# Kernel tuning notes

Hardware: AMD Instinct MI355X
Metric: run time of the kernel (lower is better)

Reference implementation:

```python
import jax, jax.numpy as jnp
import numpy as np

D_MODEL = 256
NHEAD = 8
NLAYERS = 4
B, L, K = 8, 4096, 10
EPS_ATT = 1e-6
EPS_LN = 1e-5
EPS_COS = 1e-8


def setup_inputs() -> dict:
    key = jax.random.key(0)
    ks = jax.random.split(key, 12)
    s = 1.0 / np.sqrt(D_MODEL)
    s2 = 1.0 / np.sqrt(2 * D_MODEL)
    return {
        "ClassNum": K,
        "feat": jax.random.normal(ks[0], (B, L, D_MODEL), jnp.float32),
        "feat_class": jax.random.normal(ks[1], (B, K, D_MODEL), jnp.float32),
        "Wq": jax.random.normal(ks[2], (NLAYERS, D_MODEL, D_MODEL), jnp.float32) * s,
        "Wk": jax.random.normal(ks[3], (NLAYERS, D_MODEL, D_MODEL), jnp.float32) * s,
        "Wv": jax.random.normal(ks[4], (NLAYERS, D_MODEL, D_MODEL), jnp.float32) * s,
        "Wm": jax.random.normal(ks[5], (NLAYERS, D_MODEL, D_MODEL), jnp.float32) * s,
        "W1": jax.random.normal(ks[6], (NLAYERS, 2 * D_MODEL, 2 * D_MODEL), jnp.float32) * s2,
        "W2": jax.random.normal(ks[7], (NLAYERS, 2 * D_MODEL, D_MODEL), jnp.float32) * s2,
        "g1": jnp.ones((NLAYERS, D_MODEL), jnp.float32),
        "b1": jnp.zeros((NLAYERS, D_MODEL), jnp.float32),
        "g2": jnp.ones((NLAYERS, D_MODEL), jnp.float32),
        "b2": jnp.zeros((NLAYERS, D_MODEL), jnp.float32),
    }


def _layernorm(x, g, b):
    mu = jnp.mean(x, axis=-1, keepdims=True)
    xc = x - mu
    var = jnp.mean(xc * xc, axis=-1, keepdims=True)
    return g * xc * jax.lax.rsqrt(var + EPS_LN) + b


def _encoder_layer(x, oh, Wq, Wk, Wv, Wm, W1, W2, g1, b1, g2, b2):
    # x: [B,L,C], oh: [B,L,K] one-hot cluster assignment.
    # Per-cluster LoFTR linear self-attention via segment sums (exact: the
    # per-cluster v_length scaling in LinearAttention cancels algebraically).
    bsz, seq, cdim = x.shape
    hd = cdim // NHEAD
    q = (x @ Wq).reshape(bsz, seq, NHEAD, hd)
    k = (x @ Wk).reshape(bsz, seq, NHEAD, hd)
    v = (x @ Wv).reshape(bsz, seq, NHEAD, hd)
    Q = jax.nn.elu(q) + 1.0
    Kf = jax.nn.elu(k) + 1.0
    # per-(batch,cluster) sums: KV [B,K,H,D,D], Ksum [B,K,H,D]
    KV = jnp.einsum('blc,blhd,blhe->bchde', oh, Kf, v)
    Ksum = jnp.einsum('blc,blhd->bchd', oh, Kf)
    Kt = jnp.einsum('blc,bchd->blhd', oh, Ksum)  # cluster ΣK gathered per token
    Z = 1.0 / (jnp.einsum('blhd,blhd->blh', Q, Kt) + EPS_ATT)
    msg = jnp.zeros((bsz, seq, NHEAD, hd), x.dtype)
    for c in range(oh.shape[-1]):  # small fixed ClassNum loop
        msg = msg + oh[:, :, c][:, :, None, None] * jnp.einsum(
            'blhd,bhde->blhe', Q, KV[:, c])
    msg = msg * Z[..., None]
    m = msg.reshape(bsz, seq, cdim) @ Wm
    m = _layernorm(m, g1, b1)
    h = jnp.concatenate([x, m], axis=-1) @ W1
    h = jax.nn.relu(h) @ W2
    m = _layernorm(h, g2, b2)
    return x + m


def reference(ClassNum, feat, feat_class, Wq, Wk, Wv, Wm, W1, W2, g1, b1, g2, b2):
    x = jax.lax.stop_gradient(feat)          # feat.clone().detach()
    fc = jax.lax.stop_gradient(feat_class)   # feat_class.clone().detach()
    # cosine-similarity top-1 cluster routing (torch.F.cosine_similarity, eps=1e-8)
    na = jnp.linalg.norm(fc, axis=-1)  # [B,K]
    nb = jnp.linalg.norm(x, axis=-1)   # [B,L]
    dot = jnp.einsum('bkc,blc->bkl', fc, x)
    sim = dot / jnp.maximum(na[:, :, None] * nb[:, None, :], EPS_COS)
    seg = jnp.argmax(sim, axis=1)  # [B,L] cluster id per token
    oh = jax.nn.one_hot(seg, ClassNum, dtype=x.dtype)
    for li in range(Wq.shape[0]):
        x = _encoder_layer(x, oh, Wq[li], Wk[li], Wv[li], Wm[li],
                           W1[li], W2[li], g1[li], b1[li], g2[li], b2[li])
    return x
```

## Files before the change

kernel.cpp:

```cpp
#include <hip/hip_runtime.h>
#include <hip/hip_bf16.h>
#include <math.h>

#define DM 256
#define NHEAD 8
#define HD 32
#define NL 4
#define BATCH 8
#define SEQ 4096
#define KCLS 10
#define M_TOK (BATCH*SEQ)

#define BKG 64

#define PADPOS 5120
#define NWIN (PADPOS/64)
#define KVWIN 20
#define NGRP (KVWIN*4)

using bf16x8 = __attribute__((ext_vector_type(8))) short;
using f32x4  = __attribute__((ext_vector_type(4))) float;

__device__ __forceinline__ unsigned short f2bf(float f) {
    __hip_bfloat16 b = __float2bfloat16(f);
    return __builtin_bit_cast(unsigned short, b);
}
__device__ __forceinline__ float bf2f(unsigned short u) {
    unsigned v = (unsigned)u << 16;
    return __builtin_bit_cast(float, v);
}

__device__ __forceinline__ float wave_reduce_sum(float v) {
    #pragma unroll
    for (int off = 32; off > 0; off >>= 1) v += __shfl_xor(v, off, 64);
    return v;
}

__global__ __launch_bounds__(64) void fcn_kernel(const float* __restrict__ fc,
                                                 float* __restrict__ fcn) {
    int bk = blockIdx.x;
    int lane = threadIdx.x;
    float4 fv = *(const float4*)(fc + (size_t)bk * DM + lane * 4);
    float n = fv.x*fv.x + fv.y*fv.y + fv.z*fv.z + fv.w*fv.w;
    n = wave_reduce_sum(n);
    if (lane == 0) fcn[bk] = sqrtf(n);
}

__global__ void route_kernel(const float* __restrict__ feat, const float* __restrict__ fc,
                             const float* __restrict__ fcn,
                             float* __restrict__ x, unsigned short* __restrict__ xm,
                             int* __restrict__ seg) {
    int wid = (int)((blockIdx.x * (size_t)blockDim.x + threadIdx.x) >> 6);
    int lane = threadIdx.x & 63;
    if (wid >= M_TOK) return;
    int b = wid / SEQ;
    float4 xv = *(const float4*)(feat + (size_t)wid * DM + lane * 4);
    *(float4*)(x + (size_t)wid * DM + lane * 4) = xv;
    ushort4 u; u.x = f2bf(xv.x); u.y = f2bf(xv.y); u.z = f2bf(xv.z); u.w = f2bf(xv.w);
    *(ushort4*)(xm + (size_t)wid * 512 + lane * 4) = u;
    float nb2 = xv.x*xv.x + xv.y*xv.y + xv.z*xv.z + xv.w*xv.w;
    nb2 = wave_reduce_sum(nb2);
    float nb = sqrtf(nb2);
    float best = -1e30f; int bestk = 0;
    for (int k = 0; k < KCLS; ++k) {
        float4 fv = *(const float4*)(fc + ((size_t)(b * KCLS + k)) * DM + lane * 4);
        float d = fv.x*xv.x + fv.y*xv.y + fv.z*xv.z + fv.w*xv.w;
        d = wave_reduce_sum(d);
        float sim = d / fmaxf(fcn[b * KCLS + k] * nb, 1e-8f);
        if (sim > best) { best = sim; bestk = k; }
    }
    if (lane == 0) seg[wid] = bestk;
}

__global__ __launch_bounds__(256) void seg_count(const int* __restrict__ seg,
                                                 int* __restrict__ cnt) {
    __shared__ int wc[4][KCLS];
    int b = blockIdx.x >> 4, chunk = blockIdx.x & 15;
    int t = threadIdx.x, w = t >> 6, lane = t & 63;
    int c = seg[b * SEQ + chunk * 256 + t];
    #pragma unroll
    for (int cc = 0; cc < KCLS; ++cc) {
        unsigned long long m = __ballot(c == cc);
        if (lane == 0) wc[w][cc] = __popcll(m);
    }
    __syncthreads();
    if (t < KCLS)
        cnt[(b * 16 + chunk) * KCLS + t] = wc[0][t] + wc[1][t] + wc[2][t] + wc[3][t];
}

__global__ __launch_bounds__(256) void seg_scan(const int* __restrict__ cnt,
                                                int* __restrict__ chunkbase,
                                                int* __restrict__ wseg,
                                                int* __restrict__ psegp,
                                                int* __restrict__ grange,
                                                int* __restrict__ prange,
                                                int* __restrict__ pidxp) {
    __shared__ int sTot[BATCH][KCLS];
    __shared__ int sBase[BATCH][KCLS];
    int tid = threadIdx.x;
    if (tid < BATCH * KCLS) {
        int b = tid / KCLS, c = tid % KCLS;
        int run = 0;
        #pragma unroll
        for (int j = 0; j < 16; ++j) run += cnt[(b * 16 + j) * KCLS + c];
        sTot[b][c] = run;
    }
    __syncthreads();
    if (tid < BATCH) {
        int b = tid, pb = 0;
        for (int c = 0; c < KCLS; ++c) {
            sBase[b][c] = pb;
            int psz = (sTot[b][c] + 63) & ~63;
            grange[(b * KCLS + c) * 2]     = pb >> 6;
            grange[(b * KCLS + c) * 2 + 1] = (pb + psz) >> 6;
            prange[(b * KCLS + c) * 2]     = pb + sTot[b][c];
            prange[(b * KCLS + c) * 2 + 1] = pb + psz;
            int w0 = pb >> 6, w1 = (pb + psz) >> 6;
            for (int w = w0; w < w1; ++w) wseg[b * NWIN + w] = c;
            pb += psz;
        }
        for (int w = pb >> 6; w < NWIN; ++w) wseg[b * NWIN + w] = -1;
    }
    __syncthreads();
    for (int i = tid; i < BATCH * PADPOS; i += 256) {
        int b = i / PADPOS, pos = i % PADPOS;
        int c = KCLS - 1;
        #pragma unroll
        for (int cc = KCLS - 1; cc >= 1; --cc)
            if (pos < sBase[b][cc]) c = cc - 1;
        psegp[i] = c;
        pidxp[i] = -1;
    }
    if (tid < BATCH * KCLS) {
        int b = tid / KCLS, c = tid % KCLS;
        int pre = 0;
        #pragma unroll
        for (int j = 0; j < 16; ++j) {
            chunkbase[(b * 16 + j) * KCLS + c] = sBase[b][c] + pre;
            pre += cnt[(b * 16 + j) * KCLS + c];
        }
    }
}

__global__ __launch_bounds__(256) void seg_scatter(const int* __restrict__ seg,
                                                   const int* __restrict__ chunkbase,
                                                   int* __restrict__ pidxp,
                                                   int* __restrict__ sortposG) {
    __shared__ int wc[4][KCLS];
    int b = blockIdx.x >> 4, chunk = blockIdx.x & 15;
    int t = threadIdx.x, w = t >> 6, lane = t & 63;
    int l = chunk * 256 + t;
    int c = seg[b * SEQ + l];
    int rank_w = 0;
    #pragma unroll
    for (int cc = 0; cc < KCLS; ++cc) {
        unsigned long long m = __ballot(c == cc);
        if (lane == 0) wc[w][cc] = __popcll(m);
        if (cc == c) rank_w = __popcll(m & ((1ULL << lane) - 1ULL));
    }
    __syncthreads();
    int rank = rank_w;
    for (int wp = 0; wp < 4; ++wp)
        if (wp < w) rank += wc[wp][c];
    int pos = chunkbase[(b * 16 + chunk) * KCLS + c] + rank;
    pidxp[b * PADPOS + pos] = l;
    sortposG[b * SEQ + l] = b * PADPOS + pos;
}

__global__ __launch_bounds__(256) void zero_pads(const int* __restrict__ prange,
                                                 unsigned short* __restrict__ Kb,
                                                 unsigned short* __restrict__ Vb) {
    int bc = blockIdx.x;
    int b = bc / KCLS;
    int ps = prange[bc * 2], pe = prange[bc * 2 + 1];
    int nrows = pe - ps;
    int t = threadIdx.x;
    bf16x8 z = (bf16x8){0,0,0,0,0,0,0,0};
    for (int idx = t; idx < nrows * 32; idx += 256) {
        int r = idx >> 5, c8 = (idx & 31) * 8;
        size_t row = (size_t)b * PADPOS + ps + r;
        *(bf16x8*)(Kb + row * DM + c8) = z;
        *(bf16x8*)(Vb + row * DM + c8) = z;
    }
}

__global__ __launch_bounds__(256) void transpose_all(
    const float* __restrict__ Wq, const float* __restrict__ Wk,
    const float* __restrict__ Wv, const float* __restrict__ Wm,
    const float* __restrict__ W1, const float* __restrict__ W2,
    unsigned short* __restrict__ WqkvT, unsigned short* __restrict__ WmT,
    unsigned short* __restrict__ W1T, unsigned short* __restrict__ W2T)
{
    __shared__ float s[64][65];
    int bid = blockIdx.x;
    int li = bid / 160, r = bid % 160;
    const float* src; unsigned short* dst; int K, N, kx, ny;
    if (r < 64) {
        int which = r >> 4, idx = r & 15;
        K = 256; N = 256; kx = idx & 3; ny = idx >> 2;
        if (which == 0)      { src = Wq + (size_t)li*65536; dst = WqkvT + (size_t)li*768*256; }
        else if (which == 1) { src = Wk + (size_t)li*65536; dst = WqkvT + (size_t)li*768*256 + 65536; }
        else if (which == 2) { src = Wv + (size_t)li*65536; dst = WqkvT + (size_t)li*768*256 + 131072; }
        else                 { src = Wm + (size_t)li*65536; dst = WmT + (size_t)li*65536; }
    } else if (r < 128) {
        int idx = r - 64;
        K = 512; N = 512; kx = idx & 7; ny = idx >> 3;
        src = W1 + (size_t)li*262144; dst = W1T + (size_t)li*262144;
    } else {
        int idx = r - 128;
        K = 512; N = 256; kx = idx & 7; ny = idx >> 3;
        src = W2 + (size_t)li*131072; dst = W2T + (size_t)li*131072;
    }
    int k0 = kx * 64, n0 = ny * 64;
    int t = threadIdx.x;
    int rr = t >> 4, c4 = (t & 15) * 4;
    #pragma unroll
    for (int i = 0; i < 4; ++i) {
        float4 v = *(const float4*)(src + (size_t)(k0 + rr + i*16) * N + n0 + c4);
        s[c4+0][rr+i*16] = v.x; s[c4+1][rr+i*16] = v.y;
        s[c4+2][rr+i*16] = v.z; s[c4+3][rr+i*16] = v.w;
    }
    __syncthreads();
    #pragma unroll
    for (int i = 0; i < 4; ++i) {
        int nr = rr + i*16;
        ushort4 u;
        u.x = f2bf(s[nr][c4+0]); u.y = f2bf(s[nr][c4+1]);
        u.z = f2bf(s[nr][c4+2]); u.w = f2bf(s[nr][c4+3]);
        *(ushort4*)(dst + (size_t)(n0 + nr) * K + k0 + c4) = u;
    }
}

template<int KD, int AS, int MODE>
__global__ __launch_bounds__(512, 4) void mfma_gemm(
    const unsigned short* __restrict__ A, const unsigned short* __restrict__ Bt,
    const int* __restrict__ sortpos,
    unsigned short* __restrict__ Ob0, unsigned short* __restrict__ Ob1,
    unsigned short* __restrict__ Ob2)
{
    __shared__ unsigned short As[128 * BKG];
    __shared__ unsigned short Bs[256 * BKG];
    __shared__ int sPos[128];
    int t = threadIdx.x;
    int lane = t & 63;
    int w = t >> 6;
    int wm = w & 1, wn = w >> 1;
    int li = lane & 15, lg = lane >> 4;
    int bm = blockIdx.x * 128;
    int bn = blockIdx.y * 256;

    if (MODE == 1 && t < 128) sPos[t] = sortpos[bm + t];

    f32x4 acc[4][4];
    #pragma unroll
    for (int m = 0; m < 4; ++m)
        #pragma unroll
        for (int n = 0; n < 4; ++n)
            acc[m][n] = (f32x4){0.f, 0.f, 0.f, 0.f};

    for (int k0 = 0; k0 < KD; k0 += BKG) {
        #pragma unroll
        for (int i = 0; i < 2; ++i) {
            int chunk = i * 512 + t;
            int row = chunk >> 3, cc = chunk & 7;
            int scc = cc ^ (row & 7);
            __builtin_amdgcn_global_load_lds(
                (const __attribute__((address_space(1))) void*)(A + (size_t)(bm + row) * AS + k0 + scc * 8),
                (__attribute__((address_space(3))) void*)((char*)As + chunk * 16), 16, 0, 0);
        }
        #pragma unroll
        for (int i = 0; i < 4; ++i) {
            int chunk = i * 512 + t;
            int row = chunk >> 3, cc = chunk & 7;
            int scc = cc ^ (row & 7);
            __builtin_amdgcn_global_load_lds(
                (const __attribute__((address_space(1))) void*)(Bt + (size_t)(bn + row) * KD + k0 + scc * 8),
                (__attribute__((address_space(3))) void*)((char*)Bs + chunk * 16), 16, 0, 0);
        }
        asm volatile("s_waitcnt vmcnt(0)");
        __syncthreads();
        #pragma unroll
        for (int kk = 0; kk < 2; ++kk) {
            int jc = kk * 4 + lg;
            bf16x8 af[4], bfr[4];
            #pragma unroll
            for (int m = 0; m < 4; ++m) {
                int R = wm*64 + m*16 + li;
                af[m] = *(const bf16x8*)((const char*)As + R * 128 + ((jc ^ (R & 7)) << 4));
            }
            #pragma unroll
            for (int n = 0; n < 4; ++n) {
                int R = wn*64 + n*16 + li;
                bfr[n] = *(const bf16x8*)((const char*)Bs + R * 128 + ((jc ^ (R & 7)) << 4));
            }
            #pragma unroll
            for (int m = 0; m < 4; ++m)
                #pragma unroll
                for (int n = 0; n < 4; ++n)
                    acc[m][n] = __builtin_amdgcn_mfma_f32_16x16x32_bf16(af[m], bfr[n], acc[m][n], 0, 0, 0);
        }
        __syncthreads();
    }

    int lrow0 = wm * 64 + (lane >> 4) * 4;
    int lcol = wn * 64 + (lane & 15);
    if (MODE == 1) {
        unsigned short* Obuf = (bn < 256) ? Ob0 : (bn < 512) ? Ob1 : Ob2;
        const bool act = (bn < 512);
        #pragma unroll
        for (int m = 0; m < 4; ++m)
            #pragma unroll
            for (int n = 0; n < 4; ++n)
                #pragma unroll
                for (int j = 0; j < 4; ++j) {
                    float v = acc[m][n][j];
                    if (act) v = (v > 0.f) ? v + 1.f : expf(v);
                    int drow = sPos[lrow0 + m*16 + j];
                    Obuf[(size_t)drow * 256 + lcol + n*16] = f2bf(v);
                }
    } else {
        #pragma unroll
        for (int m = 0; m < 4; ++m)
            #pragma unroll
            for (int n = 0; n < 4; ++n)
                #pragma unroll
                for (int j = 0; j < 4; ++j)
                    Ob0[(size_t)(bm + lrow0 + m*16 + j) * 512 + bn + lcol + n*16] =
                        f2bf(fmaxf(acc[m][n][j], 0.f));
    }
}

template<int KD, int LNMODE>
__global__ __launch_bounds__(256) void gemm_ln(
    const unsigned short* __restrict__ A, const unsigned short* __restrict__ Bt,
    const float* __restrict__ g, const float* __restrict__ bb,
    float* __restrict__ x, unsigned short* __restrict__ xm)
{
    __shared__ unsigned short As[64 * BKG];
    __shared__ unsigned short Bs[256 * BKG];
    __shared__ float redS[4][64];
    __shared__ float redQ[4][64];
    int t = threadIdx.x;
    int lane = t & 63;
    int w = t >> 6;
    int li = lane & 15, lg = lane >> 4;
    int bm = blockIdx.x * 64;

    f32x4 acc[4][4];
    #pragma unroll
    for (int m = 0; m < 4; ++m)
        #pragma unroll
        for (int n = 0; n < 4; ++n)
            acc[m][n] = (f32x4){0.f, 0.f, 0.f, 0.f};

    for (int k0 = 0; k0 < KD; k0 += BKG) {
        #pragma unroll
        for (int i = 0; i < 2; ++i) {
            int chunk = i * 256 + t;
            int row = chunk >> 3, cc = chunk & 7;
            int scc = cc ^ (row & 7);
            __builtin_amdgcn_global_load_lds(
                (const __attribute__((address_space(1))) void*)(A + (size_t)(bm + row) * KD + k0 + scc * 8),
                (__attribute__((address_space(3))) void*)((char*)As + chunk * 16), 16, 0, 0);
        }
        #pragma unroll
        for (int i = 0; i < 8; ++i) {
            int chunk = i * 256 + t;
            int row = chunk >> 3, cc = chunk & 7;
            int scc = cc ^ (row & 7);
            __builtin_amdgcn_global_load_lds(
                (const __attribute__((address_space(1))) void*)(Bt + (size_t)row * KD + k0 + scc * 8),
                (__attribute__((address_space(3))) void*)((char*)Bs + chunk * 16), 16, 0, 0);
        }
        asm volatile("s_waitcnt vmcnt(0)");
        __syncthreads();
        #pragma unroll
        for (int kk = 0; kk < 2; ++kk) {
            int jc = kk * 4 + lg;
            bf16x8 af[4], bfr[4];
            #pragma unroll
            for (int m = 0; m < 4; ++m) {
                int R = m*16 + li;
                af[m] = *(const bf16x8*)((const char*)As + R * 128 + ((jc ^ (R & 7)) << 4));
            }
            #pragma unroll
            for (int n = 0; n < 4; ++n) {
                int R = w*64 + n*16 + li;
                bfr[n] = *(const bf16x8*)((const char*)Bs + R * 128 + ((jc ^ (R & 7)) << 4));
            }
            #pragma unroll
            for (int m = 0; m < 4; ++m)
                #pragma unroll
                for (int n = 0; n < 4; ++n)
                    acc[m][n] = __builtin_amdgcn_mfma_f32_16x16x32_bf16(af[m], bfr[n], acc[m][n], 0, 0, 0);
        }
        __syncthreads();
    }

    float vs[4][4], vq[4][4];
    #pragma unroll
    for (int m = 0; m < 4; ++m)
        #pragma unroll
        for (int j = 0; j < 4; ++j) {
            float s = 0.f, q = 0.f;
            #pragma unroll
            for (int n = 0; n < 4; ++n) {
                float v = acc[m][n][j];
                s += v; q += v * v;
            }
            #pragma unroll
            for (int msk = 1; msk < 16; msk <<= 1) {
                s += __shfl_xor(s, msk, 64);
                q += __shfl_xor(q, msk, 64);
            }
            vs[m][j] = s; vq[m][j] = q;
        }
    if (li == 0) {
        #pragma unroll
        for (int m = 0; m < 4; ++m)
            #pragma unroll
            for (int j = 0; j < 4; ++j) {
                redS[w][m*16 + lg*4 + j] = vs[m][j];
                redQ[w][m*16 + lg*4 + j] = vq[m][j];
            }
    }
    __syncthreads();

    float gv[4], bv[4];
    #pragma unroll
    for (int n = 0; n < 4; ++n) {
        int col = w*64 + n*16 + li;
        gv[n] = g[col]; bv[n] = bb[col];
    }
    #pragma unroll
    for (int m = 0; m < 4; ++m)
        #pragma unroll
        for (int j = 0; j < 4; ++j) {
            int r = m*16 + lg*4 + j;
            float S = redS[0][r] + redS[1][r] + redS[2][r] + redS[3][r];
            float Q = redQ[0][r] + redQ[1][r] + redQ[2][r] + redQ[3][r];
            float mu = S * (1.f / 256.f);
            float var = Q * (1.f / 256.f) - mu * mu;
            float rs = rsqrtf(var + 1e-5f);
            #pragma unroll
            for (int n = 0; n < 4; ++n) {
                int col = w*64 + n*16 + li;
                float o = gv[n] * (acc[m][n][j] - mu) * rs + bv[n];
                if (LNMODE == 1) {
                    xm[(size_t)(bm + r) * 512 + 256 + col] = f2bf(o);
                } else {
                    size_t idx = (size_t)(bm + r) * 256 + col;
                    float xv = x[idx] + o;
                    x[idx] = xv;
                    xm[(size_t)(bm + r) * 512 + col] = f2bf(xv);
                }
            }
        }
}

__global__ __launch_bounds__(256) void kv_kernel(
    const unsigned short* __restrict__ Ksrt, const unsigned short* __restrict__ Vsrt,
    float* __restrict__ part)
{
    __shared__ float sK[64 * 33];
    __shared__ float sV[64 * 33];
    int blk = blockIdx.x;
    int s = blk % KVWIN;
    int bh = blk / KVWIN;
    int b = bh >> 3, h = bh & 7;
    int t = threadIdx.x;
    int d = t >> 3, e0 = (t & 7) * 4;
    int srow = t >> 2, soff = (t & 3) * 8;
    const size_t rowbase = (size_t)(b * PADPOS + s * 256);
    float* pball = part + ((size_t)bh * NGRP + s * 4) * 1056;

    for (int g = 0; g < 4; ++g) {
        size_t gsrc = (rowbase + g * 64 + srow) * DM + h * HD + soff;
        bf16x8 k8 = *(const bf16x8*)(Ksrt + gsrc);
        bf16x8 v8 = *(const bf16x8*)(Vsrt + gsrc);
        float4 ka, kb, va, vb;
        ka.x = bf2f((unsigned short)k8[0]); ka.y = bf2f((unsigned short)k8[1]);
        ka.z = bf2f((unsigned short)k8[2]); ka.w = bf2f((unsigned short)k8[3]);
        kb.x = bf2f((unsigned short)k8[4]); kb.y = bf2f((unsigned short)k8[5]);
        kb.z = bf2f((unsigned short)k8[6]); kb.w = bf2f((unsigned short)k8[7]);
        va.x = bf2f((unsigned short)v8[0]); va.y = bf2f((unsigned short)v8[1]);
        va.z = bf2f((unsigned short)v8[2]); va.w = bf2f((unsigned short)v8[3]);
        vb.x = bf2f((unsigned short)v8[4]); vb.y = bf2f((unsigned short)v8[5]);
        vb.z = bf2f((unsigned short)v8[6]); vb.w = bf2f((unsigned short)v8[7]);
        *(float4*)(sK + srow * 33 + soff)     = ka;
        *(float4*)(sK + srow * 33 + soff + 4) = kb;
        *(float4*)(sV + srow * 33 + soff)     = va;
        *(float4*)(sV + srow * 33 + soff + 4) = vb;
        __syncthreads();

        float4 a = {0.f, 0.f, 0.f, 0.f};
        float ks = 0.f;
        #pragma unroll 8
        for (int l = 0; l < 64; ++l) {
            float kd = sK[l * 33 + d];
            float4 v4 = *(const float4*)(sV + l * 33 + e0);
            a.x = fmaf(kd, v4.x, a.x);
            a.y = fmaf(kd, v4.y, a.y);
            a.z = fmaf(kd, v4.z, a.z);
            a.w = fmaf(kd, v4.w, a.w);
            ks += kd;
        }
        float* pb = pball + g * 1056;
        *(float4*)(pb + d * 32 + e0) = a;
        if ((t & 7) == 0) pb[1024 + d] = ks;
        __syncthreads();
    }
}

__global__ __launch_bounds__(256) void kv_reduce(
    const float* __restrict__ part, const int* __restrict__ grange,
    float* __restrict__ KV, float* __restrict__ Ks)
{
    int blk = blockIdx.x;
    int c = blk % KCLS;
    int bh = blk / KCLS;
    int b = bh >> 3, h = bh & 7;
    int t = threadIdx.x;
    const float* pb = part + (size_t)bh * NGRP * 1056;
    int g0 = grange[(b * KCLS + c) * 2];
    int g1 = grange[(b * KCLS + c) * 2 + 1];
    float4 acc = {0, 0, 0, 0};
    float ka = 0.f;
    for (int gg = g0; gg < g1; ++gg) {
        float4 v = *(const float4*)(pb + (size_t)gg * 1056 + t * 4);
        acc.x += v.x; acc.y += v.y; acc.z += v.z; acc.w += v.w;
        if (t < 32) ka += pb[(size_t)gg * 1056 + 1024 + t];
    }
    *(float4*)(KV + ((size_t)(b * KCLS + c) * NHEAD + h) * HD * HD + t * 4) = acc;
    if (t < 32) Ks[((size_t)(b * KCLS + c) * NHEAD + h) * HD + t] = ka;
}

__global__ __launch_bounds__(256) void msg_kernel(
    const unsigned short* __restrict__ Qs, const float* __restrict__ KV,
    const float* __restrict__ Ks, const int* __restrict__ pidxp,
    const int* __restrict__ wseg, unsigned short* __restrict__ msgb)
{
    int b = blockIdx.x / NWIN, w = blockIdx.x % NWIN;
    int c = wseg[b * NWIN + w];
    if (c < 0) return;
    __shared__ unsigned short sQ[64 * DM];
    __shared__ unsigned short kvT[NHEAD * HD * HD];
    __shared__ float sKs[NHEAD * HD];
    __shared__ float zl[64 * NHEAD];
    __shared__ int sTok[64];
    int t = threadIdx.x;
    int wv = t >> 6, lane = t & 63;

    if (t < 64) sTok[t] = pidxp[b * PADPOS + w * 64 + t];
    { int h = t >> 5, d = t & 31;
      sKs[h * HD + d] = Ks[((size_t)(b * KCLS + c) * NHEAD + h) * HD + d]; }
    const float* kvsrc = KV + (size_t)(b * KCLS + c) * NHEAD * HD * HD;
    #pragma unroll
    for (int i = 0; i < 8; ++i) {
        int q = i * 256 + t;
        float4 v = ((const float4*)kvsrc)[q];
        int g = q * 4;
        int h = g >> 10, rem = g & 1023;
        int d = rem >> 5, e = rem & 31;
        kvT[h * 1024 + (e + 0) * 32 + d] = f2bf(v.x);
        kvT[h * 1024 + (e + 1) * 32 + d] = f2bf(v.y);
        kvT[h * 1024 + (e + 2) * 32 + d] = f2bf(v.z);
        kvT[h * 1024 + (e + 3) * 32 + d] = f2bf(v.w);
    }
    const unsigned short* qsrc = Qs + (size_t)(b * PADPOS + w * 64) * DM;
    #pragma unroll
    for (int i = 0; i < 8; ++i) {
        int q = i * 256 + t;
        *(bf16x8*)(sQ + q * 8) = *(const bf16x8*)(qsrc + q * 8);
    }
    __syncthreads();

    #pragma unroll
    for (int i = 0; i < 2; ++i) {
        int idx = i * 256 + t;
        int r = idx >> 3, h = idx & 7;
        float z = 0.f;
        #pragma unroll
        for (int d8 = 0; d8 < 4; ++d8) {
            bf16x8 qv = *(const bf16x8*)(sQ + r * DM + h * 32 + d8 * 8);
            #pragma unroll
            for (int j = 0; j < 8; ++j)
                z = fmaf(bf2f((unsigned short)qv[j]), sKs[h * HD + d8 * 8 + j], z);
        }
        zl[r * NHEAD + h] = z;
    }
    __syncthreads();

    int li = lane & 15, lg = lane >> 4;
    #pragma unroll
    for (int hh = 0; hh < 2; ++hh) {
        int h = wv * 2 + hh;
        f32x4 acc[4][2];
        #pragma unroll
        for (int m = 0; m < 4; ++m)
            #pragma unroll
            for (int n = 0; n < 2; ++n)
                acc[m][n] = (f32x4){0.f, 0.f, 0.f, 0.f};
        bf16x8 bfr[2];
        #pragma unroll
        for (int n = 0; n < 2; ++n)
            bfr[n] = *(const bf16x8*)(kvT + h * 1024 + (n * 16 + li) * 32 + lg * 8);
        #pragma unroll
        for (int m = 0; m < 4; ++m) {
            bf16x8 af = *(const bf16x8*)(sQ + (m * 16 + li) * DM + h * 32 + lg * 8);
            #pragma unroll
            for (int n = 0; n < 2; ++n)
                acc[m][n] = __builtin_amdgcn_mfma_f32_16x16x32_bf16(af, bfr[n], acc[m][n], 0, 0, 0);
        }
        #pragma unroll
        for (int m = 0; m < 4; ++m)
            #pragma unroll
            for (int n = 0; n < 2; ++n)
                #pragma unroll
                for (int j = 0; j < 4; ++j) {
                    int r = m * 16 + lg * 4 + j;
                    int tok = sTok[r];
                    if (tok >= 0) {
                        float o = acc[m][n][j] / (zl[r * NHEAD + h] + 1e-6f);
                        msgb[(size_t)(b * SEQ + tok) * DM + h * 32 + n * 16 + li] = f2bf(o);
                    }
                }
    }
}

extern "C" void kernel_launch(void* const* d_in, const int* in_sizes, int n_in,
                              void* d_out, int out_size, void* d_ws, size_t ws_size,
                              hipStream_t stream)
{
    const float* feat = (const float*)d_in[1];
    const float* fc   = (const float*)d_in[2];
    const float* Wq   = (const float*)d_in[3];
    const float* Wk   = (const float*)d_in[4];
    const float* Wv   = (const float*)d_in[5];
    const float* Wm   = (const float*)d_in[6];
    const float* W1   = (const float*)d_in[7];
    const float* W2   = (const float*)d_in[8];
    const float* g1   = (const float*)d_in[9];
    const float* b1   = (const float*)d_in[10];
    const float* g2   = (const float*)d_in[11];
    const float* b2   = (const float*)d_in[12];
    float* x = (float*)d_out;

    char* ws = (char*)d_ws;
    auto alloc = [&](size_t bytes) { char* p = ws; ws += (bytes + 255) & ~(size_t)255; return p; };
    int*   seg    = (int*)  alloc((size_t)M_TOK * 4);
    int*   cnt    = (int*)  alloc((size_t)BATCH * 16 * KCLS * 4);
    int*   cbase  = (int*)  alloc((size_t)BATCH * 16 * KCLS * 4);
    int*   pidxp  = (int*)  alloc((size_t)BATCH * PADPOS * 4);
    int*   psegp  = (int*)  alloc((size_t)BATCH * PADPOS * 4);
    int*   sortposG = (int*)alloc((size_t)M_TOK * 4);
    int*   wseg   = (int*)  alloc((size_t)BATCH * NWIN * 4);
    int*   grange = (int*)  alloc((size_t)BATCH * KCLS * 2 * 4);
    int*   prange = (int*)  alloc((size_t)BATCH * KCLS * 2 * 4);
    float* fcn    = (float*)alloc((size_t)BATCH * KCLS * 4);
    float* KV     = (float*)alloc((size_t)BATCH * KCLS * NHEAD * HD * HD * 4);
    float* Ks     = (float*)alloc((size_t)BATCH * KCLS * NHEAD * HD * 4);
    unsigned short* xm = (unsigned short*)alloc((size_t)M_TOK * 512 * 2);
    char* bufA = alloc((size_t)M_TOK * 512 * 2);
    unsigned short* Qs   = (unsigned short*)alloc((size_t)BATCH * PADPOS * DM * 2);
    unsigned short* Ksrt = (unsigned short*)alloc((size_t)BATCH * PADPOS * DM * 2);
    unsigned short* Vsrt = (unsigned short*)alloc((size_t)BATCH * PADPOS * DM * 2);
    unsigned short* WqkvT = (unsigned short*)alloc((size_t)NL * 768 * 256 * 2);
    unsigned short* WmT   = (unsigned short*)alloc((size_t)NL * 256 * 256 * 2);
    unsigned short* W1T   = (unsigned short*)alloc((size_t)NL * 512 * 512 * 2);
    unsigned short* W2T   = (unsigned short*)alloc((size_t)NL * 256 * 512 * 2);

    unsigned short* hb   = (unsigned short*)bufA;
    unsigned short* msgb = (unsigned short*)bufA;
    float*          part = (float*)bufA;

    transpose_all<<<NL * 160, 256, 0, stream>>>(Wq, Wk, Wv, Wm, W1, W2,
                                                WqkvT, WmT, W1T, W2T);

    fcn_kernel<<<BATCH * KCLS, 64, 0, stream>>>(fc, fcn);
    route_kernel<<<8192, 256, 0, stream>>>(feat, fc, fcn, x, xm, seg);

    seg_count<<<BATCH * 16, 256, 0, stream>>>(seg, cnt);
    seg_scan<<<1, 256, 0, stream>>>(cnt, cbase, wseg, psegp, grange, prange, pidxp);
    seg_scatter<<<BATCH * 16, 256, 0, stream>>>(seg, cbase, pidxp, sortposG);
    zero_pads<<<BATCH * KCLS, 256, 0, stream>>>(prange, Ksrt, Vsrt);

    for (int li = 0; li < NL; ++li) {
        const unsigned short* wqkv = WqkvT + (size_t)li * 768 * 256;
        const unsigned short* wm   = WmT + (size_t)li * 65536;
        const unsigned short* w1   = W1T + (size_t)li * 262144;
        const unsigned short* w2   = W2T + (size_t)li * 131072;

        mfma_gemm<256, 512, 1><<<dim3(256, 3), 512, 0, stream>>>(xm, wqkv, sortposG, Qs, Ksrt, Vsrt);

        kv_kernel<<<BATCH * NHEAD * KVWIN, 256, 0, stream>>>(Ksrt, Vsrt, part);
        kv_reduce<<<BATCH * NHEAD * KCLS, 256, 0, stream>>>(part, grange, KV, Ks);

        msg_kernel<<<BATCH * NWIN, 256, 0, stream>>>(Qs, KV, Ks, pidxp, wseg, msgb);

        gemm_ln<256, 1><<<512, 256, 0, stream>>>(msgb, wm, g1 + li * DM, b1 + li * DM, nullptr, xm);

        mfma_gemm<512, 512, 2><<<dim3(256, 2), 512, 0, stream>>>(xm, w1, nullptr, hb, nullptr, nullptr);

        gemm_ln<512, 2><<<512, 256, 0, stream>>>(hb, w2, g2 + li * DM, b2 + li * DM, x, xm);
    }
}
```

Measured before the change: 646.9 us.

## Double-buffer LDS tiles in MFMA GEMM to overlap global loads with compute

Turns the GEMM's single shared-memory A/B tiles into two ping-pong buffers. The next K-slice is loaded straight into LDS while MFMAs run on the current slice, with one barrier per step instead of two. This is meant to hide global-load latency behind compute. It doubles LDS use per block (about 96KB+), which may cut the number of resident blocks below the launch-bounds target of 4.

```diff
diff --git a/kernel.cpp b/kernel.cpp
--- a/kernel.cpp
+++ b/kernel.cpp
@@ -238,8 +238,8 @@
     unsigned short* __restrict__ Ob0, unsigned short* __restrict__ Ob1,
     unsigned short* __restrict__ Ob2)
 {
-    __shared__ unsigned short As[128 * BKG];
-    __shared__ unsigned short Bs[256 * BKG];
+    __shared__ unsigned short As[2][128 * BKG];
+    __shared__ unsigned short Bs[2][256 * BKG];
     __shared__ int sPos[128];
     int t = threadIdx.x;
     int lane = t & 63;
@@ -258,7 +258,7 @@
         for (int n = 0; n < 4; ++n)
             acc[m][n] = (f32x4){0.f, 0.f, 0.f, 0.f};
 
-    for (int k0 = 0; k0 < KD; k0 += BKG) {
+    auto STAGE = [&](int buf, int k0) {
         #pragma unroll
         for (int i = 0; i < 2; ++i) {
             int chunk = i * 512 + t;
@@ -266,7 +266,7 @@
             int scc = cc ^ (row & 7);
             __builtin_amdgcn_global_load_lds(
                 (const __attribute__((address_space(1))) void*)(A + (size_t)(bm + row) * AS + k0 + scc * 8),
-                (__attribute__((address_space(3))) void*)((char*)As + chunk * 16), 16, 0, 0);
+                (__attribute__((address_space(3))) void*)((char*)&As[buf][0] + chunk * 16), 16, 0, 0);
         }
         #pragma unroll
         for (int i = 0; i < 4; ++i) {
@@ -275,10 +275,20 @@
             int scc = cc ^ (row & 7);
             __builtin_amdgcn_global_load_lds(
                 (const __attribute__((address_space(1))) void*)(Bt + (size_t)(bn + row) * KD + k0 + scc * 8),
-                (__attribute__((address_space(3))) void*)((char*)Bs + chunk * 16), 16, 0, 0);
-        }
-        asm volatile("s_waitcnt vmcnt(0)");
-        __syncthreads();
+                (__attribute__((address_space(3))) void*)((char*)&Bs[buf][0] + chunk * 16), 16, 0, 0);
+        }
+    };
+
+    constexpr int NSTEP = KD / BKG;
+    STAGE(0, 0);
+    asm volatile("s_waitcnt vmcnt(0)" ::: "memory");
+    __builtin_amdgcn_s_barrier();
+    int cur = 0;
+    #pragma unroll
+    for (int step = 0; step < NSTEP; ++step) {
+        if (step + 1 < NSTEP) STAGE(cur ^ 1, (step + 1) * BKG);
+        const char* Ab = (const char*)&As[cur][0];
+        const char* Bb = (const char*)&Bs[cur][0];
         #pragma unroll
         for (int kk = 0; kk < 2; ++kk) {
             int jc = kk * 4 + lg;
@@ -286,12 +296,12 @@
             #pragma unroll
             for (int m = 0; m < 4; ++m) {
                 int R = wm*64 + m*16 + li;
-                af[m] = *(const bf16x8*)((const char*)As + R * 128 + ((jc ^ (R & 7)) << 4));
+                af[m] = *(const bf16x8*)(Ab + R * 128 + ((jc ^ (R & 7)) << 4));
             }
             #pragma unroll
             for (int n = 0; n < 4; ++n) {
                 int R = wn*64 + n*16 + li;
-                bfr[n] = *(const bf16x8*)((const char*)Bs + R * 128 + ((jc ^ (R & 7)) << 4));
+                bfr[n] = *(const bf16x8*)(Bb + R * 128 + ((jc ^ (R & 7)) << 4));
             }
             #pragma unroll
             for (int m = 0; m < 4; ++m)
@@ -299,7 +309,10 @@
                 for (int n = 0; n < 4; ++n)
                     acc[m][n] = __builtin_amdgcn_mfma_f32_16x16x32_bf16(af[m], bfr[n], acc[m][n], 0, 0, 0);
         }
-        __syncthreads();
+        asm volatile("s_waitcnt vmcnt(0) lgkmcnt(0)" ::: "memory");
+        __builtin_amdgcn_sched_barrier(0);
+        __builtin_amdgcn_s_barrier();
+        cur ^= 1;
     }
 
     int lrow0 = wm * 64 + (lane >> 4) * 4;
```

After: 736.7 us. 1.14x slower.
